# Performance work log

Measured on AMD Instinct MI355X. Metric: run time of the kernel, lower is better.

The kernel has to match this reference:

```python
import jax, jax.numpy as jnp
import numpy as np

B, S, HID = 1, 2048, 2048
NH = 16
QL, KVL = 1536, 512
DN, DR, DV = 128, 64, 128
DQ = DN + DR  # 192
IH, ID = 4, 128
TOPK = 1024
EPS = 1e-6
THETA = 10000.0


def rope_interleaved(x, cos, sin):
    # x: (b,s,h,d); cos/sin: (s,d//2); pairs are (x[...,2i], x[...,2i+1])
    xr = x[..., 0::2]
    xi = x[..., 1::2]
    c = cos[None, :, None, :]
    s = sin[None, :, None, :]
    yr = xr * c - xi * s
    yi = xr * s + xi * c
    return jnp.stack([yr, yi], axis=-1).reshape(x.shape)


def rope_noninterleaved(x, cos, sin):
    # rotate-half style: pairs are (x[...,i], x[...,i+d/2])
    d = x.shape[-1] // 2
    x1, x2 = x[..., :d], x[..., d:]
    c = cos[None, :, None, :]
    s = sin[None, :, None, :]
    return jnp.concatenate([x1 * c - x2 * s, x1 * s + x2 * c], axis=-1)


def rmsnorm(x, w):
    var = jnp.mean(x * x, axis=-1, keepdims=True)
    return w * (x * jax.lax.rsqrt(var + EPS))


def layernorm(x, g, b):
    mu = jnp.mean(x, axis=-1, keepdims=True)
    var = jnp.mean((x - mu) ** 2, axis=-1, keepdims=True)
    return (x - mu) * jax.lax.rsqrt(var + EPS) * g + b


def setup_inputs() -> dict:
    key = jax.random.key(0)
    ks = jax.random.split(key, 12)
    std = 0.02
    x = jax.random.normal(ks[0], (B, S, HID), jnp.float32)
    pos = jnp.arange(S, dtype=jnp.float32)
    inv_freq = THETA ** (-jnp.arange(0, DR, 2, dtype=jnp.float32) / DR)
    ang = pos[:, None] * inv_freq[None, :]  # (S, DR//2)
    cos, sin = jnp.cos(ang), jnp.sin(ang)
    mask = jnp.where(jnp.tril(jnp.ones((S, S), bool)), 0.0, -1e9).astype(jnp.float32)
    return {
        "x": x, "cos": cos, "sin": sin, "mask": mask,
        "Wq_a": jax.random.normal(ks[1], (HID, QL), jnp.float32) * std,
        "q_norm_w": jnp.ones((QL,), jnp.float32),
        "Wq_b": jax.random.normal(ks[2], (QL, NH * DQ), jnp.float32) * std,
        "Wkv_a": jax.random.normal(ks[3], (HID, KVL + DR), jnp.float32) * std,
        "kv_norm_w": jnp.ones((KVL,), jnp.float32),
        "Wkv_b": jax.random.normal(ks[4], (KVL, NH * (DN + DV)), jnp.float32) * std,
        "Wo": jax.random.normal(ks[5], (NH * DV, HID), jnp.float32) * std,
        "IWq_b": jax.random.normal(ks[6], (QL, IH * ID), jnp.float32) * std,
        "IWk": jax.random.normal(ks[7], (HID, ID), jnp.float32) * std,
        "Ik_norm_w": jnp.ones((ID,), jnp.float32),
        "Ik_norm_b": jnp.zeros((ID,), jnp.float32),
        "IWproj": jax.random.normal(ks[8], (HID, IH), jnp.float32) * std,
    }


def indexer(x, qr, cos, sin, mask, IWq_b, IWk, Ik_norm_w, Ik_norm_b, IWproj):
    b, s, _ = x.shape
    q = (qr @ IWq_b).reshape(b, s, IH, ID)
    q_pe, q_nope = q[..., :DR], q[..., DR:]
    q_pe = rope_noninterleaved(q_pe, cos, sin)
    q = jnp.concatenate([q_pe, q_nope], axis=-1)
    k = layernorm(x @ IWk, Ik_norm_w, Ik_norm_b)  # (b,s,ID)
    k_pe = rope_noninterleaved(k[:, :, None, :DR], cos, sin)[:, :, 0]
    k = jnp.concatenate([k_pe, k[..., DR:]], axis=-1)
    weights = (x @ IWproj) * (IH ** -0.5) * (ID ** -0.5)  # (b,s,IH)
    logits = jax.nn.relu(jnp.einsum('bthd,bsd->btsh', q, k))
    index_score = jnp.einsum('btsh,bth->bts', logits, weights)
    index_score = index_score + mask[None]
    k_top = min(TOPK, s)
    topk_idx = jax.lax.top_k(index_score, k_top)[1]  # (b,s,k)
    bi = jnp.arange(b)[:, None, None]
    si = jnp.arange(s)[None, :, None]
    index_mask = jnp.full((b, s, s), -1e9, jnp.float32).at[bi, si, topk_idx].set(0.0)
    return index_mask


def reference(x, cos, sin, mask, Wq_a, q_norm_w, Wq_b, Wkv_a, kv_norm_w, Wkv_b, Wo,
              IWq_b, IWk, Ik_norm_w, Ik_norm_b, IWproj):
    b, s, _ = x.shape
    qr = rmsnorm(x @ Wq_a, q_norm_w)  # (b,s,QL)
    q = (qr @ Wq_b).reshape(b, s, NH, DQ)
    q_nope, q_pe = q[..., :DN], q[..., DN:]
    q_pe = rope_interleaved(q_pe, cos, sin)
    q = jnp.concatenate([q_nope, q_pe], axis=-1)
    kv_full = x @ Wkv_a
    kv, k_pe = kv_full[..., :KVL], kv_full[..., KVL:]
    kv = rmsnorm(kv, kv_norm_w)
    k_pe = rope_interleaved(k_pe[:, :, None, :], cos, sin)  # (b,s,1,DR)
    kv_exp = (kv @ Wkv_b).reshape(b, s, NH, DN + DV)
    k_nope, v = kv_exp[..., :DN], kv_exp[..., DN:]
    k = jnp.concatenate([k_nope, jnp.broadcast_to(k_pe, (b, s, NH, DR))], axis=-1)
    scores = jnp.einsum('bshd,bthd->bsht', q, k) * (DQ ** -0.5)
    index_mask = indexer(x, qr, cos, sin, mask, IWq_b, IWk, Ik_norm_w, Ik_norm_b, IWproj)
    scores = scores + index_mask[:, :, None, :] + mask[None, :, None, :]
    probs = jax.nn.softmax(scores, axis=-1)
    out = jnp.einsum('bsht,bthd->bshd', probs, v).reshape(b, s, NH * DV)
    return out @ Wo
```

## Files before the change

kernel.cpp:

```cpp
#include <hip/hip_runtime.h>
#include <math.h>
#include <stdint.h>

#define S 2048
#define HID 2048
#define NH 16
#define QL 1536
#define KVL 512
#define DN 128
#define DR 64
#define DV 128
#define DQ 192
#define IH 4
#define ID 128
#define TOPK 1024

#define N1 2244
#define N2 3584

#define CDIV(a,b) (((a)+(b)-1)/(b))

typedef float f32x4 __attribute__((ext_vector_type(4)));
typedef short bf16x8 __attribute__((ext_vector_type(8)));

__device__ __forceinline__ ushort f2b(float f) {
    uint32_t u = __float_as_uint(f);
    u += 0x7fffu + ((u >> 16) & 1u);
    return (ushort)(u >> 16);
}

#define GLL16(g, l)                                                            \
    __builtin_amdgcn_global_load_lds(                                          \
        (const __attribute__((address_space(1))) void*)(g),                    \
        (__attribute__((address_space(3))) void*)(l), 16, 0, 0)

__global__ __launch_bounds__(256) void gemm_bt(const ushort* __restrict__ A,
                                               const ushort* __restrict__ BT,
                                               float* __restrict__ C,
                                               int M, int N, int K) {
    __shared__ ushort As[128 * 32];
    __shared__ ushort Bs[128 * 32];
    const int tid = threadIdx.x;
    const int w = tid >> 6, l = tid & 63;
    const int quad = l >> 4, lane = l & 15;
    const int row0 = blockIdx.y * 128, col0 = blockIdx.x * 128;
    const int wr = (w >> 1) * 64, wc = (w & 1) * 64;
    f32x4 acc[4][4];
#pragma unroll
    for (int i = 0; i < 4; i++)
#pragma unroll
        for (int j = 0; j < 4; j++) acc[i][j] = (f32x4)0.f;

    const int srow = w * 32 + (l >> 2);
    const int c8 = (l & 3) * 8;
    const ushort* pa0 = A + (size_t)(row0 + srow) * K + c8;
    const ushort* pa1 = A + (size_t)(row0 + srow + 16) * K + c8;
    int bn0 = col0 + srow;      if (bn0 > N - 1) bn0 = N - 1;
    int bn1 = col0 + srow + 16; if (bn1 > N - 1) bn1 = N - 1;
    const ushort* pb0 = BT + (size_t)bn0 * K + c8;
    const ushort* pb1 = BT + (size_t)bn1 * K + c8;
    ushort* sa0 = As + srow * 32 + c8;
    ushort* sa1 = sa0 + 16 * 32;
    ushort* sb0 = Bs + srow * 32 + c8;
    ushort* sb1 = sb0 + 16 * 32;

    for (int k0 = 0; k0 < K; k0 += 32) {
        __syncthreads();
        GLL16(pa0 + k0, sa0);
        GLL16(pa1 + k0, sa1);
        GLL16(pb0 + k0, sb0);
        GLL16(pb1 + k0, sb1);
        __syncthreads();
        bf16x8 af[4], bf[4];
#pragma unroll
        for (int mi = 0; mi < 4; mi++)
            af[mi] = *(const bf16x8*)(As + (wr + mi * 16 + lane) * 32 + quad * 8);
#pragma unroll
        for (int ni = 0; ni < 4; ni++)
            bf[ni] = *(const bf16x8*)(Bs + (wc + ni * 16 + lane) * 32 + quad * 8);
#pragma unroll
        for (int mi = 0; mi < 4; mi++)
#pragma unroll
            for (int ni = 0; ni < 4; ni++)
                acc[mi][ni] = __builtin_amdgcn_mfma_f32_16x16x32_bf16(af[mi], bf[ni], acc[mi][ni], 0, 0, 0);
    }
#pragma unroll
    for (int mi = 0; mi < 4; mi++)
#pragma unroll
        for (int ni = 0; ni < 4; ni++)
#pragma unroll
            for (int r = 0; r < 4; r++) {
                int row = row0 + wr + mi * 16 + quad * 4 + r;
                int col = col0 + wc + ni * 16 + lane;
                if (col < N) C[(size_t)row * N + col] = acc[mi][ni][r];
            }
}

__global__ __launch_bounds__(256) void gemm_bt_h(const ushort* __restrict__ A,
                                                 const ushort* __restrict__ BT,
                                                 ushort* __restrict__ C,
                                                 int M, int N, int K) {
    __shared__ ushort As[128 * 32];
    __shared__ ushort Bs[128 * 32];
    const int tid = threadIdx.x;
    const int w = tid >> 6, l = tid & 63;
    const int quad = l >> 4, lane = l & 15;
    const int row0 = blockIdx.y * 128, col0 = blockIdx.x * 128;
    const int wr = (w >> 1) * 64, wc = (w & 1) * 64;
    f32x4 acc[4][4];
#pragma unroll
    for (int i = 0; i < 4; i++)
#pragma unroll
        for (int j = 0; j < 4; j++) acc[i][j] = (f32x4)0.f;

    const int srow = w * 32 + (l >> 2);
    const int c8 = (l & 3) * 8;
    const ushort* pa0 = A + (size_t)(row0 + srow) * K + c8;
    const ushort* pa1 = A + (size_t)(row0 + srow + 16) * K + c8;
    int bn0 = col0 + srow;      if (bn0 > N - 1) bn0 = N - 1;
    int bn1 = col0 + srow + 16; if (bn1 > N - 1) bn1 = N - 1;
    const ushort* pb0 = BT + (size_t)bn0 * K + c8;
    const ushort* pb1 = BT + (size_t)bn1 * K + c8;
    ushort* sa0 = As + srow * 32 + c8;
    ushort* sa1 = sa0 + 16 * 32;
    ushort* sb0 = Bs + srow * 32 + c8;
    ushort* sb1 = sb0 + 16 * 32;

    for (int k0 = 0; k0 < K; k0 += 32) {
        __syncthreads();
        GLL16(pa0 + k0, sa0);
        GLL16(pa1 + k0, sa1);
        GLL16(pb0 + k0, sb0);
        GLL16(pb1 + k0, sb1);
        __syncthreads();
        bf16x8 af[4], bf[4];
#pragma unroll
        for (int mi = 0; mi < 4; mi++)
            af[mi] = *(const bf16x8*)(As + (wr + mi * 16 + lane) * 32 + quad * 8);
#pragma unroll
        for (int ni = 0; ni < 4; ni++)
            bf[ni] = *(const bf16x8*)(Bs + (wc + ni * 16 + lane) * 32 + quad * 8);
#pragma unroll
        for (int mi = 0; mi < 4; mi++)
#pragma unroll
            for (int ni = 0; ni < 4; ni++)
                acc[mi][ni] = __builtin_amdgcn_mfma_f32_16x16x32_bf16(af[mi], bf[ni], acc[mi][ni], 0, 0, 0);
    }
#pragma unroll
    for (int mi = 0; mi < 4; mi++)
#pragma unroll
        for (int ni = 0; ni < 4; ni++)
#pragma unroll
            for (int r = 0; r < 4; r++) {
                int row = row0 + wr + mi * 16 + quad * 4 + r;
                int col = col0 + wc + ni * 16 + lane;
                if (col < N) C[(size_t)row * N + col] = f2b(acc[mi][ni][r]);
            }
}

__device__ __forceinline__ void wtrans_body(const float* W, ushort* WT, int K, int N,
                                            int k0, int n0) {
    __shared__ float t[64][65];
    int rr = threadIdx.x >> 6, cc = threadIdx.x & 63;
#pragma unroll
    for (int p = 0; p < 16; p++) {
        int k = k0 + p * 4 + rr, n = n0 + cc;
        t[p * 4 + rr][cc] = (k < K && n < N) ? W[(size_t)k * N + n] : 0.f;
    }
    __syncthreads();
#pragma unroll
    for (int p = 0; p < 16; p++) {
        int n = n0 + p * 4 + rr, k = k0 + cc;
        if (n < N && k < K) WT[(size_t)n * K + k] = f2b(t[cc][p * 4 + rr]);
    }
}

__global__ __launch_bounds__(256) void wtrans(const float* __restrict__ W, ushort* __restrict__ WT,
                                              int K, int N) {
    wtrans_body(W, WT, K, N, blockIdx.x * 64, blockIdx.y * 64);
}

__global__ __launch_bounds__(256) void wtrans_c1(const float* __restrict__ W0, const float* __restrict__ W1,
                                                 const float* __restrict__ W2, const float* __restrict__ W3,
                                                 ushort* __restrict__ WT) {
    int yb = blockIdx.y;
    const float* W; int N; size_t off; int y;
    if (yb < 24)      { W = W0; N = 1536; off = 0;                      y = yb; }
    else if (yb < 33) { W = W1; N = 576;  off = (size_t)1536 * HID;     y = yb - 24; }
    else if (yb < 35) { W = W2; N = 128;  off = (size_t)2112 * HID;     y = yb - 33; }
    else              { W = W3; N = 4;    off = (size_t)2240 * HID;     y = yb - 35; }
    wtrans_body(W, WT + off, HID, N, blockIdx.x * 64, y * 64);
}

__global__ __launch_bounds__(256) void wtrans_c2(const float* __restrict__ W0, const float* __restrict__ W1,
                                                 ushort* __restrict__ WT) {
    int yb = blockIdx.y;
    const float* W; int N; size_t off; int y;
    if (yb < 48) { W = W0; N = 3072; off = 0;                  y = yb; }
    else         { W = W1; N = 512;  off = (size_t)3072 * QL;  y = yb - 48; }
    wtrans_body(W, WT + off, QL, N, blockIdx.x * 64, y * 64);
}

__global__ void cvt_bf16(const float* __restrict__ in, ushort* __restrict__ out) {
    int i = blockIdx.x * 256 + threadIdx.x;
    float4 v = *(const float4*)(in + (size_t)i * 4);
    uint32_t lo = (uint32_t)f2b(v.x) | ((uint32_t)f2b(v.y) << 16);
    uint32_t hi = (uint32_t)f2b(v.z) | ((uint32_t)f2b(v.w) << 16);
    *(uint2*)(out + (size_t)i * 4) = make_uint2(lo, hi);
}

__global__ __launch_bounds__(256) void post_c1(const float* __restrict__ C1,
                                               const float* __restrict__ qw,
                                               const float* __restrict__ kvw,
                                               const float* __restrict__ ikg,
                                               const float* __restrict__ ikb,
                                               const float* __restrict__ cosb,
                                               const float* __restrict__ sinb,
                                               ushort* __restrict__ qrb,
                                               ushort* __restrict__ kvnb,
                                               float* __restrict__ kpe,
                                               float* __restrict__ kiT) {
    const int t = blockIdx.x, tid = threadIdx.x;
    const float* row = C1 + (size_t)t * N1;
    __shared__ float red[256];
    __shared__ float kis[128];
    float ss = 0.f;
    for (int i = tid; i < 1536; i += 256) { float v = row[i]; ss += v * v; }
    red[tid] = ss; __syncthreads();
    for (int st = 128; st > 0; st >>= 1) { if (tid < st) red[tid] += red[tid + st]; __syncthreads(); }
    float sq = rsqrtf(red[0] / 1536.f + 1e-6f);
    __syncthreads();
    float s2 = 0.f;
    for (int i = tid; i < 512; i += 256) { float v = row[1536 + i]; s2 += v * v; }
    red[tid] = s2; __syncthreads();
    for (int st = 128; st > 0; st >>= 1) { if (tid < st) red[tid] += red[tid + st]; __syncthreads(); }
    float skv = rsqrtf(red[0] / 512.f + 1e-6f);
    __syncthreads();
    float kv_ = (tid < 128) ? row[2112 + tid] : 0.f;
    red[tid] = kv_; __syncthreads();
    for (int st = 128; st > 0; st >>= 1) { if (tid < st) red[tid] += red[tid + st]; __syncthreads(); }
    float mu = red[0] / 128.f;
    __syncthreads();
    red[tid] = kv_ * kv_; __syncthreads();
    for (int st = 128; st > 0; st >>= 1) { if (tid < st) red[tid] += red[tid + st]; __syncthreads(); }
    float var = red[0] / 128.f - mu * mu;
    for (int i = tid; i < 1536; i += 256) qrb[(size_t)t * QL + i] = f2b(row[i] * sq * qw[i]);
    for (int i = tid; i < 512; i += 256)  kvnb[(size_t)t * KVL + i] = f2b(row[1536 + i] * skv * kvw[i]);
    if (tid < 32) {
        float c = cosb[t * 32 + tid], s = sinb[t * 32 + tid];
        float xr = row[2048 + 2 * tid], xi = row[2048 + 2 * tid + 1];
        kpe[t * 64 + 2 * tid]     = xr * c - xi * s;
        kpe[t * 64 + 2 * tid + 1] = xr * s + xi * c;
    }
    if (tid < 128) kis[tid] = (kv_ - mu) * rsqrtf(var + 1e-6f) * ikg[tid] + ikb[tid];
    __syncthreads();
    if (tid < 128) {
        float outv;
        if (tid < 32) {
            float c = cosb[t * 32 + tid], s = sinb[t * 32 + tid];
            outv = kis[tid] * c - kis[tid + 32] * s;
        } else if (tid < 64) {
            int j = tid - 32;
            float c = cosb[t * 32 + j], s = sinb[t * 32 + j];
            outv = kis[j] * s + kis[tid] * c;
        } else {
            outv = kis[tid];
        }
        kiT[(size_t)tid * S + t] = outv;
    }
}

__global__ __launch_bounds__(256) void post_c2(float* __restrict__ C2,
                                               const float* __restrict__ cosb,
                                               const float* __restrict__ sinb,
                                               ushort* __restrict__ qb) {
    const int t = blockIdx.x, tid = threadIdx.x;
    __shared__ float cs[32], sn[32];
    if (tid < 32) { cs[tid] = cosb[t * 32 + tid]; sn[tid] = sinb[t * 32 + tid]; }
    __syncthreads();
    const float sc = 0.10412775370051047f;
    const float* src0 = C2 + (size_t)t * N2;
    for (int i = tid; i < NH * 96; i += 256) {
        int h = i / 96, p = i % 96;
        const float* src = src0 + h * 192;
        ushort* dst = qb + ((size_t)h * S + t) * 192;
        if (p < 64) {
            dst[2 * p]     = f2b(src[2 * p] * sc);
            dst[2 * p + 1] = f2b(src[2 * p + 1] * sc);
        } else {
            int j = p - 64;
            float c = cs[j], s = sn[j];
            float xr = src[128 + 2 * j], xi = src[128 + 2 * j + 1];
            dst[128 + 2 * j]     = f2b((xr * c - xi * s) * sc);
            dst[128 + 2 * j + 1] = f2b((xr * s + xi * c) * sc);
        }
    }
    if (tid < 128) {
        int h = tid >> 5, j = tid & 31;
        float* p = C2 + (size_t)t * N2 + 3072 + h * 128;
        float c = cs[j], s = sn[j];
        float x1 = p[j], x2 = p[j + 32];
        p[j] = x1 * c - x2 * s;
        p[j + 32] = x1 * s + x2 * c;
    }
}

__global__ __launch_bounds__(256) void pack_kv(const ushort* __restrict__ kvexp_h,
                                               const float* __restrict__ kpe,
                                               ushort* __restrict__ kb,
                                               ushort* __restrict__ vT) {
    __shared__ ushort t[64][136];
    const int s0 = blockIdx.x * 64, h = blockIdx.y, tid = threadIdx.x;
    const int row = tid >> 2, c = tid & 3;
    const ushort* src = kvexp_h + (size_t)(s0 + row) * 4096 + h * 256;
    ushort* kbr = kb + ((size_t)h * S + s0 + row) * 192;
#pragma unroll
    for (int i = 0; i < 4; i++) {
        int off = c * 32 + i * 8;
        *(uint4*)(kbr + off) = *(const uint4*)(src + off);
        *(uint4*)(&t[row][off]) = *(const uint4*)(src + 128 + off);
    }
    const float* kp = kpe + (size_t)(s0 + row) * 64 + c * 16;
#pragma unroll
    for (int i = 0; i < 16; i++) kbr[128 + c * 16 + i] = f2b(kp[i]);
    __syncthreads();
    const int d = tid >> 1, sh = (tid & 1) * 32;
    ushort* dst = vT + ((size_t)h * 128 + d) * S + s0 + sh;
#pragma unroll
    for (int i = 0; i < 32; i++) dst[i] = t[sh + i][d];
}

__global__ __launch_bounds__(256) void iscore4(const float* __restrict__ qi,
                                               const float* __restrict__ kiT,
                                               const float* __restrict__ iw,
                                               float* __restrict__ iscore) {
    int t = blockIdx.x;
    int s0 = blockIdx.y * 1024;
    if (s0 > t) return;
    int s = s0 + threadIdx.x * 4;
    __shared__ float qs[4 * ID];
    __shared__ float ws4[4];
    for (int i = threadIdx.x; i < 4 * ID; i += 256) qs[i] = qi[(size_t)t * N2 + i];
    if (threadIdx.x < 4) ws4[threadIdx.x] = iw[(size_t)t * N1 + threadIdx.x] * 0.04419417382415922f;
    __syncthreads();
    if (s > t) return;
    float a[4][4];
#pragma unroll
    for (int h = 0; h < 4; h++)
#pragma unroll
        for (int c = 0; c < 4; c++) a[h][c] = 0.f;
    for (int d = 0; d < ID; d++) {
        float4 kv = *(const float4*)(kiT + (size_t)d * S + s);
#pragma unroll
        for (int h = 0; h < 4; h++) {
            float qv = qs[h * ID + d];
            a[h][0] += qv * kv.x; a[h][1] += qv * kv.y;
            a[h][2] += qv * kv.z; a[h][3] += qv * kv.w;
        }
    }
#pragma unroll
    for (int c = 0; c < 4; c++) {
        if (s + c > t) break;
        float sc = fmaxf(a[0][c], 0.f) * ws4[0] + fmaxf(a[1][c], 0.f) * ws4[1] +
                   fmaxf(a[2][c], 0.f) * ws4[2] + fmaxf(a[3][c], 0.f) * ws4[3];
        iscore[(size_t)t * S + s + c] = sc;
    }
}

__device__ inline unsigned sortable_u32(float f) {
    unsigned u = __float_as_uint(f);
    return (u & 0x80000000u) ? ~u : (u | 0x80000000u);
}

__global__ __launch_bounds__(256) void topk_mask(const float* __restrict__ iscore,
                                                 uint32_t* __restrict__ msk) {
    int t = blockIdx.x, tid = threadIdx.x;
    uint32_t* mrow = msk + (size_t)t * 64;
    if (t < TOPK) {
        if (tid < 64) {
            int full = (t + 1) >> 5;
            uint32_t wv2 = (tid < full) ? 0xFFFFFFFFu : 0u;
            if (tid == full) { int rem = (t + 1) & 31; wv2 = rem ? ((1u << rem) - 1u) : 0u; }
            mrow[tid] = wv2;
        }
        return;
    }
    const float* row = iscore + (size_t)t * S;
    const int n = t + 1;
    const int wv = tid >> 6;
    __shared__ int hist[4][256];
    __shared__ int scan[256];
    __shared__ int bsel, ksel;
    __shared__ uint32_t bytes[256];

    int jb = tid * 8;
    float4 v0 = *(const float4*)(row + jb);
    float4 v1 = *(const float4*)(row + jb + 4);
    uint32_t lsu[8];
    {
        float vvv[8] = {v0.x, v0.y, v0.z, v0.w, v1.x, v1.y, v1.z, v1.w};
#pragma unroll
        for (int i = 0; i < 8; i++)
            lsu[i] = (jb + i < n) ? sortable_u32(vvv[i]) : 0u;
    }
    unsigned prefix = 0, prefmask = 0;
    int k = TOPK;
    for (int pass = 0; pass < 4; pass++) {
        int shift = 24 - pass * 8;
#pragma unroll
        for (int r = 0; r < 4; r++) hist[r][tid] = 0;
        __syncthreads();
#pragma unroll
        for (int i = 0; i < 8; i++) {
            uint32_t u = lsu[i];
            if ((u & prefmask) == prefix) atomicAdd(&hist[wv][(u >> shift) & 255], 1);
        }
        __syncthreads();
        int h = hist[0][tid] + hist[1][tid] + hist[2][tid] + hist[3][tid];
        scan[tid] = h; __syncthreads();
        for (int st = 1; st < 256; st <<= 1) {
            int a = scan[tid];
            int b = (tid + st < 256) ? scan[tid + st] : 0;
            __syncthreads();
            scan[tid] = a + b;
            __syncthreads();
        }
        int snext = (tid < 255) ? scan[tid + 1] : 0;
        if (scan[tid] >= k && snext < k) { bsel = tid; ksel = k - snext; }
        __syncthreads();
        prefix |= ((unsigned)bsel) << shift;
        prefmask |= 0xFFu << shift;
        k = ksel;
        __syncthreads();
    }
    const unsigned u_thr = prefix;
    const int need = k;
    uint32_t gtbits = 0, eqbits = 0;
    int eqcnt = 0;
#pragma unroll
    for (int i = 0; i < 8; i++) {
        uint32_t u = lsu[i];
        if (u > u_thr) gtbits |= 1u << i;
        else if (u == u_thr) { eqbits |= 1u << i; eqcnt++; }
    }
    scan[tid] = eqcnt; __syncthreads();
    for (int st = 1; st < 256; st <<= 1) {
        int a = scan[tid];
        int b = (tid >= st) ? scan[tid - st] : 0;
        __syncthreads();
        scan[tid] = a + b;
        __syncthreads();
    }
    int room = need - (scan[tid] - eqcnt);
    uint32_t keep = 0;
#pragma unroll
    for (int i = 0; i < 8; i++)
        if ((eqbits >> i) & 1u) { if (room > 0) { keep |= 1u << i; room--; } }
    bytes[tid] = gtbits | keep;
    __syncthreads();
    if (tid < 64)
        mrow[tid] = bytes[tid * 4] | (bytes[tid * 4 + 1] << 8) |
                    (bytes[tid * 4 + 2] << 16) | (bytes[tid * 4 + 3] << 24);
}

__global__ __launch_bounds__(256, 2) void fattn6(const ushort* __restrict__ qb,
                                                 const ushort* __restrict__ kb,
                                                 const ushort* __restrict__ vT,
                                                 const uint32_t* __restrict__ msk,
                                                 float* __restrict__ Opart,
                                                 float* __restrict__ mlbuf) {
    __shared__ ushort Ks[24 * 512];
    __shared__ ushort Vs[16 * 512];
    __shared__ ushort Pm[4][16 * 72];
    const int tid = threadIdx.x;
    const int w = tid >> 6, l = tid & 63, quad = l >> 4, lane = l & 15;
    const int b = blockIdx.x;
    const int r8 = b & 7, j = b >> 3;
    const int h = r8 + 8 * (j & 1);
    const int idx = j >> 1;
    const int pair = idx & 15, part = idx >> 4;
    const int ta = pair, tb = 31 - pair, nA = ta + 1;
    const int vlo = part * 11, vhi = vlo + 11;
    const int qa0 = ta * 64, qb0 = tb * 64;

    bf16x8 qfa[6], qfb[6];
    {
        const ushort* qpa = qb + ((size_t)h * S + qa0 + w * 16 + lane) * 192;
        const ushort* qpb = qb + ((size_t)h * S + qb0 + w * 16 + lane) * 192;
#pragma unroll
        for (int ks = 0; ks < 6; ks++) {
            qfa[ks] = *(const bf16x8*)(qpa + ks * 32 + quad * 8);
            qfb[ks] = *(const bf16x8*)(qpb + ks * 32 + quad * 8);
        }
    }
    f32x4 oa[8], ob[8];
#pragma unroll
    for (int i = 0; i < 8; i++) { oa[i] = (f32x4)0.f; ob[i] = (f32x4)0.f; }
    float ma[4], la[4], mb[4], lb[4];
#pragma unroll
    for (int r = 0; r < 4; r++) { ma[r] = -1e30f; la[r] = 0.f; mb[r] = -1e30f; lb[r] = 0.f; }

    ushort* pw = &Pm[w][0];
    const ushort* kbase = kb + (size_t)h * S * 192;
    const ushort* vbase = vT + (size_t)h * 128 * S;

    for (int kt = 0; kt <= tb; kt++) {
        const int idxB = (kt <= ta) ? 2 * kt : kt + nA;
        const int hasA = (kt <= ta);
        const int idxA = 2 * kt + 1;
        const bool doB = (idxB >= vlo && idxB < vhi);
        const bool doA = hasA && (idxA >= vlo && idxA < vhi);
        if (!(doA || doB)) continue;
        const int s0 = kt * 64;
        __syncthreads();
#pragma unroll
        for (int ii = 0; ii < 6; ii++) {
            const int i = w * 6 + ii;
            const int ks = i >> 2, kq = i & 3;
            const ushort* src = kbase + (size_t)(s0 + kq * 16 + lane) * 192 + ks * 32 + quad * 8;
            GLL16(src, Ks + i * 512 + l * 8);
        }
#pragma unroll
        for (int ii = 0; ii < 4; ii++) {
            const int i = w * 4 + ii;
            const int k2 = i >> 3, nt = i & 7;
            const ushort* src = vbase + (size_t)(nt * 16 + lane) * S + s0 + k2 * 32 + quad * 8;
            GLL16(src, Vs + i * 512 + l * 8);
        }
        __syncthreads();

#pragma unroll
        for (int pass = 0; pass < 2; pass++) {
            if (pass == 0 && !doA) continue;
            if (pass == 1 && !doB) continue;
            const bf16x8* qf = (pass == 0) ? qfa : qfb;
            f32x4* oacc      = (pass == 0) ? oa : ob;
            float* mm        = (pass == 0) ? ma : mb;
            float* ll        = (pass == 0) ? la : lb;
            const int q0t    = (pass == 0) ? qa0 : qb0;

            f32x4 sc[4];
#pragma unroll
            for (int kq = 0; kq < 4; kq++) {
                sc[kq] = (f32x4)0.f;
#pragma unroll
                for (int ks = 0; ks < 6; ks++) {
                    bf16x8 bfr = *(const bf16x8*)(Ks + (ks * 4 + kq) * 512 + quad * 128 + lane * 8);
                    sc[kq] = __builtin_amdgcn_mfma_f32_16x16x32_bf16(qf[ks], bfr, sc[kq], 0, 0, 0);
                }
            }
            uint32_t w0[4], w1[4];
            {
                const int rowbase = q0t + w * 16 + quad * 4;
#pragma unroll
                for (int r = 0; r < 4; r++) {
                    const uint32_t* mp = msk + (size_t)(rowbase + r) * 64 + (s0 >> 5);
                    w0[r] = mp[0]; w1[r] = mp[1];
                }
            }
            float vmax[4] = {-1e30f, -1e30f, -1e30f, -1e30f};
#pragma unroll
            for (int kq = 0; kq < 4; kq++) {
                const int sh = (kq & 1) * 16 + lane;
#pragma unroll
                for (int r = 0; r < 4; r++) {
                    uint32_t word = (kq < 2) ? w0[r] : w1[r];
                    float v = ((word >> sh) & 1u) ? sc[kq][r] : -1e30f;
                    sc[kq][r] = v;
                    vmax[r] = fmaxf(vmax[r], v);
                }
            }
#pragma unroll
            for (int off = 1; off < 16; off <<= 1)
#pragma unroll
                for (int r = 0; r < 4; r++)
                    vmax[r] = fmaxf(vmax[r], __shfl_xor(vmax[r], off, 64));
            float alpha[4], psum[4];
#pragma unroll
            for (int r = 0; r < 4; r++) {
                float mnew = fmaxf(mm[r], vmax[r]);
                alpha[r] = exp2f(mm[r] - mnew);
                mm[r] = mnew;
                psum[r] = 0.f;
            }
#pragma unroll
            for (int kq = 0; kq < 4; kq++)
#pragma unroll
                for (int r = 0; r < 4; r++) {
                    float v = sc[kq][r];
                    float e = (v < -1e29f) ? 0.f : exp2f(v - mm[r]);
                    psum[r] += e;
                    pw[(quad * 4 + r) * 72 + kq * 16 + lane] = f2b(e);
                }
#pragma unroll
            for (int off = 1; off < 16; off <<= 1)
#pragma unroll
                for (int r = 0; r < 4; r++)
                    psum[r] += __shfl_xor(psum[r], off, 64);
#pragma unroll
            for (int r = 0; r < 4; r++) ll[r] = ll[r] * alpha[r] + psum[r];

            bf16x8 pfr[2];
#pragma unroll
            for (int k2 = 0; k2 < 2; k2++)
                pfr[k2] = *(const bf16x8*)(pw + lane * 72 + k2 * 32 + quad * 8);
#pragma unroll
            for (int nt = 0; nt < 8; nt++) {
#pragma unroll
                for (int r = 0; r < 4; r++) oacc[nt][r] *= alpha[r];
#pragma unroll
                for (int k2 = 0; k2 < 2; k2++) {
                    bf16x8 vfr = *(const bf16x8*)(Vs + ((k2 * 8 + nt) * 4 + quad) * 128 + lane * 8);
                    oacc[nt] = __builtin_amdgcn_mfma_f32_16x16x32_bf16(pfr[k2], vfr, oacc[nt], 0, 0, 0);
                }
            }
        }
    }
#pragma unroll
    for (int pass = 0; pass < 2; pass++) {
        const f32x4* oacc = (pass == 0) ? oa : ob;
        const float* mm   = (pass == 0) ? ma : mb;
        const float* ll   = (pass == 0) ? la : lb;
        const int qt      = (pass == 0) ? ta : tb;
        float* Op = Opart + (size_t)((qt * 16 + h) * 3 + part) * (64 * 128);
        float* mlp = mlbuf + (size_t)((qt * 16 + h) * 3 + part) * 128;
#pragma unroll
        for (int nt = 0; nt < 8; nt++)
#pragma unroll
            for (int r = 0; r < 4; r++)
                Op[(w * 16 + quad * 4 + r) * 128 + nt * 16 + lane] = oacc[nt][r];
        if (lane == 0) {
#pragma unroll
            for (int r = 0; r < 4; r++) {
                mlp[(w * 16 + quad * 4 + r) * 2 + 0] = mm[r];
                mlp[(w * 16 + quad * 4 + r) * 2 + 1] = ll[r];
            }
        }
    }
}

__global__ __launch_bounds__(256) void attn_combine(const float* __restrict__ Opart,
                                                    const float* __restrict__ mlbuf,
                                                    ushort* __restrict__ attn_b) {
    const int qt = blockIdx.x, h = blockIdx.y, tid = threadIdx.x;
    const size_t base = ((size_t)qt * 16 + h) * 3;
    const float* Op0 = Opart + base * 8192;
    const float* Op1 = Op0 + 8192;
    const float* Op2 = Op1 + 8192;
    const float* ml0 = mlbuf + base * 128;
    const float* ml1 = ml0 + 128;
    const float* ml2 = ml1 + 128;
#pragma unroll
    for (int i = 0; i < 32; i++) {
        int id = tid + i * 256;
        int row = id >> 7, d = id & 127;
        float m0 = ml0[row * 2], l0 = ml0[row * 2 + 1];
        float m1 = ml1[row * 2], l1 = ml1[row * 2 + 1];
        float m2 = ml2[row * 2], l2 = ml2[row * 2 + 1];
        float m = fmaxf(fmaxf(m0, m1), m2);
        float e0 = exp2f(m0 - m), e1 = exp2f(m1 - m), e2 = exp2f(m2 - m);
        float linv = 1.f / (l0 * e0 + l1 * e1 + l2 * e2);
        float v = (Op0[id] * e0 + Op1[id] * e1 + Op2[id] * e2) * linv;
        attn_b[(size_t)(qt * 64 + row) * 2048 + h * 128 + d] = f2b(v);
    }
}

extern "C" void kernel_launch(void* const* d_in, const int* in_sizes, int n_in,
                              void* d_out, int out_size, void* d_ws, size_t ws_size,
                              hipStream_t stream) {
    const float* x        = (const float*)d_in[0];
    const float* cosb     = (const float*)d_in[1];
    const float* sinb     = (const float*)d_in[2];
    const float* Wq_a     = (const float*)d_in[4];
    const float* q_norm_w = (const float*)d_in[5];
    const float* Wq_b     = (const float*)d_in[6];
    const float* Wkv_a    = (const float*)d_in[7];
    const float* kv_norm_w= (const float*)d_in[8];
    const float* Wkv_b    = (const float*)d_in[9];
    const float* Wo       = (const float*)d_in[10];
    const float* IWq_b    = (const float*)d_in[11];
    const float* IWk      = (const float*)d_in[12];
    const float* Ik_norm_w= (const float*)d_in[13];
    const float* Ik_norm_b= (const float*)d_in[14];
    const float* IWproj   = (const float*)d_in[15];
    float* out = (float*)d_out;

    char* ws = (char*)d_ws;
    size_t o = 0;
    auto take = [&](size_t b) { char* p = ws + o; o += (b + 255) & ~(size_t)255; return p; };
    ushort* xb     = (ushort*)take((size_t)S * HID * 2);
    ushort* qrb    = (ushort*)take((size_t)S * QL * 2);
    ushort* qb     = (ushort*)take((size_t)NH * S * DQ * 2);
    ushort* kvnb   = (ushort*)take((size_t)S * KVL * 2);
    float*  kpe    = (float*)take((size_t)S * DR * 4);
    ushort* kb     = (ushort*)take((size_t)NH * S * DQ * 2);
    ushort* vT     = (ushort*)take((size_t)NH * DV * S * 2);
    uint32_t* msk  = (uint32_t*)take((size_t)S * 64 * 4);
    float*  mlbuf  = (float*)take((size_t)32 * 16 * 3 * 64 * 2 * 4);
    ushort* WTp    = (ushort*)take((size_t)N2 * QL * 2);
    float*  C1     = (float*)take((size_t)S * N1 * 4);
    char*   big    = take((size_t)32 * 16 * 3 * 8192 * 4 + 1024);
    ushort* kvexp_h= (ushort*)take((size_t)S * 4096 * 2);
    float*  kiT    = (float*)take((size_t)128 * S * 4);
    char*   poolb  = take((size_t)16777216);

    float* C2     = (float*)big;
    float* Opart  = (float*)big;
    float* iscore = (float*)poolb;
    ushort* attn_b = (ushort*)poolb;

    cvt_bf16<<<(S * HID) / 1024, 256, 0, stream>>>(x, xb);

    wtrans_c1<<<dim3(32, 36), 256, 0, stream>>>(Wq_a, Wkv_a, IWk, IWproj, WTp);
    gemm_bt<<<dim3(CDIV(N1, 128), S / 128), 256, 0, stream>>>(xb, WTp, C1, S, N1, HID);
    post_c1<<<S, 256, 0, stream>>>(C1, q_norm_w, kv_norm_w, Ik_norm_w, Ik_norm_b,
                                   cosb, sinb, qrb, kvnb, kpe, kiT);

    wtrans_c2<<<dim3(24, 56), 256, 0, stream>>>(Wq_b, IWq_b, WTp);
    gemm_bt<<<dim3(N2 / 128, S / 128), 256, 0, stream>>>(qrb, WTp, C2, S, N2, QL);
    post_c2<<<S, 256, 0, stream>>>(C2, cosb, sinb, qb);

    wtrans<<<dim3(8, 64), 256, 0, stream>>>(Wkv_b, WTp, KVL, NH * (DN + DV));
    gemm_bt_h<<<dim3(32, S / 128), 256, 0, stream>>>(kvnb, WTp, kvexp_h, S, NH * (DN + DV), KVL);
    pack_kv<<<dim3(S / 64, NH), 256, 0, stream>>>(kvexp_h, kpe, kb, vT);

    iscore4<<<dim3(S, S / 1024), 256, 0, stream>>>(C2 + 3072, kiT, C1 + 2240, iscore);
    topk_mask<<<S, 256, 0, stream>>>(iscore, msk);

    fattn6<<<768, 256, 0, stream>>>(qb, kb, vT, msk, Opart, mlbuf);
    attn_combine<<<dim3(32, 16), 256, 0, stream>>>(Opart, mlbuf, attn_b);

    wtrans<<<dim3(32, 32), 256, 0, stream>>>(Wo, WTp, NH * DV, HID);
    gemm_bt<<<dim3(HID / 128, S / 128), 256, 0, stream>>>(attn_b, WTp, out, S, HID, NH * DV);

    (void)in_sizes; (void)n_in; (void)out_size; (void)ws_size; (void)o;
}
```

Before: 537.2 us.

## Double-buffer LDS tiles in bf16 GEMM kernels to overlap loads with MFMA

Both GEMM kernels now use two LDS buffers per operand. Each iteration issues the global-to-LDS loads for the next K tile before running the MFMAs on the current tile, which replaces the two barriers per iteration with one wait plus one barrier. The goal is to hide global memory latency behind compute. LDS use per block doubles, which may reduce occupancy.

```diff
diff --git a/kernel.cpp b/kernel.cpp
--- a/kernel.cpp
+++ b/kernel.cpp
@@ -38,8 +38,8 @@
                                                const ushort* __restrict__ BT,
                                                float* __restrict__ C,
                                                int M, int N, int K) {
-    __shared__ ushort As[128 * 32];
-    __shared__ ushort Bs[128 * 32];
+    __shared__ ushort As[2][128 * 32];
+    __shared__ ushort Bs[2][128 * 32];
     const int tid = threadIdx.x;
     const int w = tid >> 6, l = tid & 63;
     const int quad = l >> 4, lane = l & 15;
@@ -59,30 +59,39 @@
     int bn1 = col0 + srow + 16; if (bn1 > N - 1) bn1 = N - 1;
     const ushort* pb0 = BT + (size_t)bn0 * K + c8;
     const ushort* pb1 = BT + (size_t)bn1 * K + c8;
-    ushort* sa0 = As + srow * 32 + c8;
-    ushort* sa1 = sa0 + 16 * 32;
-    ushort* sb0 = Bs + srow * 32 + c8;
-    ushort* sb1 = sb0 + 16 * 32;
-
+    const int soff = srow * 32 + c8;
+
+    GLL16(pa0, &As[0][soff]);
+    GLL16(pa1, &As[0][soff + 16 * 32]);
+    GLL16(pb0, &Bs[0][soff]);
+    GLL16(pb1, &Bs[0][soff + 16 * 32]);
+    asm volatile("s_waitcnt vmcnt(0)" ::: "memory");
+    __builtin_amdgcn_s_barrier();
+
+    int cur = 0;
     for (int k0 = 0; k0 < K; k0 += 32) {
-        __syncthreads();
-        GLL16(pa0 + k0, sa0);
-        GLL16(pa1 + k0, sa1);
-        GLL16(pb0 + k0, sb0);
-        GLL16(pb1 + k0, sb1);
-        __syncthreads();
+        const int nxt = cur ^ 1;
+        if (k0 + 32 < K) {
+            GLL16(pa0 + k0 + 32, &As[nxt][soff]);
+            GLL16(pa1 + k0 + 32, &As[nxt][soff + 16 * 32]);
+            GLL16(pb0 + k0 + 32, &Bs[nxt][soff]);
+            GLL16(pb1 + k0 + 32, &Bs[nxt][soff + 16 * 32]);
+        }
         bf16x8 af[4], bf[4];
 #pragma unroll
         for (int mi = 0; mi < 4; mi++)
-            af[mi] = *(const bf16x8*)(As + (wr + mi * 16 + lane) * 32 + quad * 8);
+            af[mi] = *(const bf16x8*)(&As[cur][(wr + mi * 16 + lane) * 32 + quad * 8]);
 #pragma unroll
         for (int ni = 0; ni < 4; ni++)
-            bf[ni] = *(const bf16x8*)(Bs + (wc + ni * 16 + lane) * 32 + quad * 8);
+            bf[ni] = *(const bf16x8*)(&Bs[cur][(wc + ni * 16 + lane) * 32 + quad * 8]);
 #pragma unroll
         for (int mi = 0; mi < 4; mi++)
 #pragma unroll
             for (int ni = 0; ni < 4; ni++)
                 acc[mi][ni] = __builtin_amdgcn_mfma_f32_16x16x32_bf16(af[mi], bf[ni], acc[mi][ni], 0, 0, 0);
+        asm volatile("s_waitcnt vmcnt(0)" ::: "memory");
+        __builtin_amdgcn_s_barrier();
+        cur = nxt;
     }
 #pragma unroll
     for (int mi = 0; mi < 4; mi++)
@@ -100,8 +109,8 @@
                                                  const ushort* __restrict__ BT,
                                                  ushort* __restrict__ C,
                                                  int M, int N, int K) {
-    __shared__ ushort As[128 * 32];
-    __shared__ ushort Bs[128 * 32];
+    __shared__ ushort As[2][128 * 32];
+    __shared__ ushort Bs[2][128 * 32];
     const int tid = threadIdx.x;
     const int w = tid >> 6, l = tid & 63;
     const int quad = l >> 4, lane = l & 15;
@@ -121,30 +130,39 @@
     int bn1 = col0 + srow + 16; if (bn1 > N - 1) bn1 = N - 1;
     const ushort* pb0 = BT + (size_t)bn0 * K + c8;
     const ushort* pb1 = BT + (size_t)bn1 * K + c8;
-    ushort* sa0 = As + srow * 32 + c8;
-    ushort* sa1 = sa0 + 16 * 32;
-    ushort* sb0 = Bs + srow * 32 + c8;
-    ushort* sb1 = sb0 + 16 * 32;
-
+    const int soff = srow * 32 + c8;
+
+    GLL16(pa0, &As[0][soff]);
+    GLL16(pa1, &As[0][soff + 16 * 32]);
+    GLL16(pb0, &Bs[0][soff]);
+    GLL16(pb1, &Bs[0][soff + 16 * 32]);
+    asm volatile("s_waitcnt vmcnt(0)" ::: "memory");
+    __builtin_amdgcn_s_barrier();
+
+    int cur = 0;
     for (int k0 = 0; k0 < K; k0 += 32) {
-        __syncthreads();
-        GLL16(pa0 + k0, sa0);
-        GLL16(pa1 + k0, sa1);
-        GLL16(pb0 + k0, sb0);
-        GLL16(pb1 + k0, sb1);
-        __syncthreads();
+        const int nxt = cur ^ 1;
+        if (k0 + 32 < K) {
+            GLL16(pa0 + k0 + 32, &As[nxt][soff]);
+            GLL16(pa1 + k0 + 32, &As[nxt][soff + 16 * 32]);
+            GLL16(pb0 + k0 + 32, &Bs[nxt][soff]);
+            GLL16(pb1 + k0 + 32, &Bs[nxt][soff + 16 * 32]);
+        }
         bf16x8 af[4], bf[4];
 #pragma unroll
         for (int mi = 0; mi < 4; mi++)
-            af[mi] = *(const bf16x8*)(As + (wr + mi * 16 + lane) * 32 + quad * 8);
+            af[mi] = *(const bf16x8*)(&As[cur][(wr + mi * 16 + lane) * 32 + quad * 8]);
 #pragma unroll
         for (int ni = 0; ni < 4; ni++)
-            bf[ni] = *(const bf16x8*)(Bs + (wc + ni * 16 + lane) * 32 + quad * 8);
+            bf[ni] = *(const bf16x8*)(&Bs[cur][(wc + ni * 16 + lane) * 32 + quad * 8]);
 #pragma unroll
         for (int mi = 0; mi < 4; mi++)
 #pragma unroll
             for (int ni = 0; ni < 4; ni++)
                 acc[mi][ni] = __builtin_amdgcn_mfma_f32_16x16x32_bf16(af[mi], bf[ni], acc[mi][ni], 0, 0, 0);
+        asm volatile("s_waitcnt vmcnt(0)" ::: "memory");
+        __builtin_amdgcn_s_barrier();
+        cur = nxt;
     }
 #pragma unroll
     for (int mi = 0; mi < 4; mi++)
```

Result: faster. 514.9 us (-4.1%).
